# Kernel optimization log

Measured on AMD Instinct MI355X. Metric: run time of the kernel, lower is better.

The kernel has to match this reference:

```python
import jax, jax.numpy as jnp
import numpy as np

D_MODEL = 1024
N_HEADS = 16
D_HEAD = D_MODEL // N_HEADS


def setup_inputs() -> dict:
    key = jax.random.key(0)
    ks = jax.random.split(key, 16)
    B, S, D = 2, 2048, D_MODEL
    s = 1.0 / np.sqrt(D)
    inp = {
        "query": jax.random.normal(ks[0], (B, S, D), jnp.float32),
        "key": jax.random.normal(ks[1], (B, S, D), jnp.float32),
        "value": jax.random.normal(ks[2], (B, S, D), jnp.float32),
        "pos_embedding": jax.random.normal(ks[3], (B, S, D), jnp.float32),
        "Wq": jax.random.normal(ks[4], (D, D), jnp.float32) * s,
        "bq": jnp.zeros((D,), jnp.float32),
        "Wk": jax.random.normal(ks[5], (D, D), jnp.float32) * s,
        "bk": jnp.zeros((D,), jnp.float32),
        "Wv": jax.random.normal(ks[6], (D, D), jnp.float32) * s,
        "bv": jnp.zeros((D,), jnp.float32),
        "Wpos": jax.random.normal(ks[7], (D, D), jnp.float32) * s,
        "u_bias": jax.random.normal(ks[8], (N_HEADS, D_HEAD), jnp.float32) * s,
        "v_bias": jax.random.normal(ks[9], (N_HEADS, D_HEAD), jnp.float32) * s,
        "Wout": jax.random.normal(ks[10], (D, D), jnp.float32) * s,
        "bout": jnp.zeros((D,), jnp.float32),
    }
    return inp


def _rel_shift(pos_score):
    # Transformer-XL relative shift: pad one zero column, reshape, drop first row.
    B, H, S1, S2 = pos_score.shape
    zeros = jnp.zeros((B, H, S1, 1), pos_score.dtype)
    padded = jnp.concatenate([zeros, pos_score], axis=-1)  # [B,H,S1,S2+1]
    padded = padded.reshape(B, H, S2 + 1, S1)
    return padded[:, :, 1:].reshape(B, H, S1, S2)


def reference(query, key, value, pos_embedding, Wq, bq, Wk, bk, Wv, bv, Wpos, u_bias, v_bias, Wout, bout):
    B, S, D = query.shape
    H, dh = N_HEADS, D_HEAD
    q = (query @ Wq + bq).reshape(B, S, H, dh)            # [B,S,H,dh]
    k = (key @ Wk + bk).reshape(B, S, H, dh)              # [B,S,H,dh]
    v = (value @ Wv + bv).reshape(B, S, H, dh)            # [B,S,H,dh]
    p = (pos_embedding @ Wpos).reshape(B, S, H, dh)       # [B,S,H,dh]

    content_score = jnp.einsum('bqhd,bkhd->bhqk', q + u_bias, k)
    pos_score = jnp.einsum('bqhd,bkhd->bhqk', q + v_bias, p)
    pos_score = _rel_shift(pos_score)

    score = (content_score + pos_score) / jnp.asarray(np.sqrt(D), score_dtype := content_score.dtype)
    attn = jax.nn.softmax(score, axis=-1)                 # [B,H,S,S]
    context = jnp.einsum('bhqk,bkhd->bqhd', attn, v).reshape(B, S, D)
    out = context @ Wout + bout
    return out, attn
```

## Files before the change

### kernel.cpp

```cpp
#include <hip/hip_runtime.h>

#define S_LEN 2048
#define DM    1024
#define NH    16
#define DH    64
#define BATCH 2
#define S2    ((size_t)S_LEN * S_LEN)

typedef _Float16 half_t;
typedef _Float16 f16x8 __attribute__((ext_vector_type(8)));
typedef _Float16 f16x4 __attribute__((ext_vector_type(4)));
typedef float    f32x4 __attribute__((ext_vector_type(4)));

__device__ __forceinline__ void gll16(const void* g, void* l) {
  __builtin_amdgcn_global_load_lds(
      (const __attribute__((address_space(1))) void*)g,
      (__attribute__((address_space(3))) void*)l, 16, 0, 0);
}

__device__ __forceinline__ void stage_gll(half_t* lds, const half_t* src, int stride) {
  const int t = threadIdx.x, w = t >> 6, lane = t & 63;
  const int c1 = lane & 7, r8 = lane >> 3;
#pragma unroll
  for (int it = 0; it < 4; ++it) {
    int r = w * 32 + it * 8 + r8;
    const half_t* g = src + (size_t)r * stride + ((c1 ^ r8) << 3);
    gll16(g, lds + (size_t)w * 2048 + it * 512);
  }
}

__device__ __forceinline__ void mfma_block(const half_t* At, const half_t* Bt,
                                           int w, int lane, f32x4 acc[2][8]) {
  const int grp = lane >> 4, li = lane & 15;
#pragma unroll
  for (int ks = 0; ks < 2; ++ks) {
    const int chunk = ks * 4 + grp;
    f16x8 a[2], b[8];
#pragma unroll
    for (int fr = 0; fr < 2; ++fr) {
      int r = w * 32 + fr * 16 + li;
      a[fr] = *(const f16x8*)&At[(size_t)(r * 8 + (chunk ^ (r & 7))) * 8];
    }
#pragma unroll
    for (int fc = 0; fc < 8; ++fc) {
      int r = fc * 16 + li;
      b[fc] = *(const f16x8*)&Bt[(size_t)(r * 8 + (chunk ^ (r & 7))) * 8];
    }
#pragma unroll
    for (int fr = 0; fr < 2; ++fr)
#pragma unroll
      for (int fc = 0; fc < 8; ++fc)
        acc[fr][fc] = __builtin_amdgcn_mfma_f32_16x16x32_f16(a[fr], b[fc], acc[fr][fc], 0, 0, 0);
  }
}

template<typename ST>
__device__ __forceinline__ void load8s(const ST* p, float* o) {
  if constexpr (sizeof(ST) == 2) {
    f16x8 v = *(const f16x8*)p;
#pragma unroll
    for (int e = 0; e < 8; ++e) o[e] = (float)v[e];
  } else {
    const float4* q = (const float4*)p;
    float4 a = q[0], b = q[1];
    o[0]=a.x; o[1]=a.y; o[2]=a.z; o[3]=a.w; o[4]=b.x; o[5]=b.y; o[6]=b.z; o[7]=b.w;
  }
}

struct AArgs { const float* src[4]; half_t* dst[4]; };

__global__ __launch_bounds__(256) void a2h(AArgs a, half_t* zbuf) {
  if (blockIdx.x == 0 && blockIdx.y == 0 && threadIdx.x < 8) {
    float4 z = {0.f, 0.f, 0.f, 0.f};
    ((float4*)zbuf)[threadIdx.x] = z;
  }
  const float* s = a.src[blockIdx.y];
  half_t* d = a.dst[blockIdx.y];
  size_t i = ((size_t)blockIdx.x * 256 + threadIdx.x) * 8;
  float4 v0 = *(const float4*)(s + i), v1 = *(const float4*)(s + i + 4);
  f16x8 h;
  h[0]=(half_t)v0.x; h[1]=(half_t)v0.y; h[2]=(half_t)v0.z; h[3]=(half_t)v0.w;
  h[4]=(half_t)v1.x; h[5]=(half_t)v1.y; h[6]=(half_t)v1.z; h[7]=(half_t)v1.w;
  *(f16x8*)(d + i) = h;
}

struct WArgs { const float* src[5]; half_t* dst[5]; };

__global__ __launch_bounds__(256) void wconv(WArgs wa) {
  __shared__ float T[64][65];
  const float* W = wa.src[blockIdx.z];
  half_t* D = wa.dst[blockIdx.z];
  const int k0 = blockIdx.x * 64, n0 = blockIdx.y * 64;
  const int t = threadIdx.x;
#pragma unroll
  for (int it = 0; it < 4; ++it) {
    int idx = t + it * 256; int r = idx >> 4, c4 = (idx & 15) * 4;
    float4 v = *(const float4*)(W + (size_t)(k0 + r) * DM + n0 + c4);
    T[r][c4] = v.x; T[r][c4 + 1] = v.y; T[r][c4 + 2] = v.z; T[r][c4 + 3] = v.w;
  }
  __syncthreads();
#pragma unroll
  for (int it = 0; it < 2; ++it) {
    int idx = t + it * 256; int n = idx >> 3, kc = (idx & 7) * 8;
    f16x8 o;
#pragma unroll
    for (int e = 0; e < 8; ++e) o[e] = (half_t)T[kc + e][n];
    *(f16x8*)&D[(size_t)(n0 + n) * DM + k0 + kc] = o;
  }
}

struct GArgs {
  const half_t* A[4];  const half_t* Bt[4];
  const float* ba[4]; const float* bu[4]; const float* bv[4];
  half_t* oa[4]; half_t* ob[4]; float* of[4];
};

template<bool F32OUT>
__global__ __launch_bounds__(256) void gemm_k(GArgs g, int K) {
  __shared__ __align__(16) half_t At[2][128 * 64];
  __shared__ __align__(16) half_t Bt[2][128 * 64];
  const int z = blockIdx.z;
  const half_t* A = g.A[z];
  const half_t* B = g.Bt[z];
  const int n0 = blockIdx.x * 128, m0 = blockIdx.y * 128;
  const int t = threadIdx.x, w = t >> 6, lane = t & 63;
  const f32x4 zf = {0.f, 0.f, 0.f, 0.f};
  f32x4 acc[2][8];
#pragma unroll
  for (int i = 0; i < 2; ++i)
#pragma unroll
    for (int j = 0; j < 8; ++j) acc[i][j] = zf;

  stage_gll(At[0], A + (size_t)m0 * K, K);
  stage_gll(Bt[0], B + (size_t)n0 * K, K);
  __syncthreads();
  int cur = 0;
  for (int k0 = 0; k0 < K; k0 += 64) {
    int nk = k0 + 64;
    if (nk < K) {
      stage_gll(At[cur ^ 1], A + (size_t)m0 * K + nk, K);
      stage_gll(Bt[cur ^ 1], B + (size_t)n0 * K + nk, K);
    }
    mfma_block(At[cur], Bt[cur], w, lane, acc);
    __syncthreads();
    cur ^= 1;
  }
  const int grp = lane >> 4, li = lane & 15;
#pragma unroll
  for (int fr = 0; fr < 2; ++fr)
#pragma unroll
    for (int fc = 0; fc < 8; ++fc)
#pragma unroll
      for (int r = 0; r < 4; ++r) {
        int row = m0 + w * 32 + fr * 16 + grp * 4 + r;
        int col = n0 + fc * 16 + li;
        float v = acc[fr][fc][r];
        if (g.ba[z]) v += g.ba[z][col];
        if constexpr (F32OUT) {
          g.of[z][(size_t)row * DM + col] = v;
        } else {
          float v1 = v + (g.bu[z] ? g.bu[z][col] : 0.f);
          g.oa[z][(size_t)row * DM + col] = (half_t)v1;
          if (g.ob[z]) g.ob[z][(size_t)row * DM + col] = (half_t)(v + g.bv[z][col]);
        }
      }
}

__global__ __launch_bounds__(256) void vtrans(const half_t* vp, half_t* vT) {
  __shared__ half_t T[64][72];
  const int s0 = blockIdx.x * 64, h = blockIdx.y, b = blockIdx.z;
  const int t = threadIdx.x;
#pragma unroll
  for (int it = 0; it < 2; ++it) {
    int idx = t + it * 256; int s = idx >> 3, c = idx & 7;
    uint4 v = *(const uint4*)(vp + ((size_t)(b * S_LEN + s0 + s)) * DM + h * DH + c * 8);
    *(uint4*)&T[s][c * 8] = v;
  }
  __syncthreads();
  half_t* dst = vT + ((size_t)(b * NH + h)) * DH * S_LEN;
#pragma unroll
  for (int it = 0; it < 2; ++it) {
    int idx = t + it * 256; int d = idx >> 3, sc = (idx & 7) * 8;
    f16x8 o;
#pragma unroll
    for (int e = 0; e < 8; ++e) o[e] = T[sc + e][d];
    *(f16x8*)&dst[(size_t)d * S_LEN + s0 + sc] = o;
  }
}

template<typename ST>
__global__ __launch_bounds__(512, 4) void score_fused(
    const half_t* __restrict__ qu_, const half_t* __restrict__ qv_,
    const half_t* __restrict__ kp_, const half_t* __restrict__ pp_,
    const half_t* __restrict__ zbuf, ST* __restrict__ sc, float* __restrict__ part)
{
  __shared__ __align__(16) half_t RegA[32768];
  __shared__ __align__(16) half_t QV[128 * 64];
  half_t* QU = RegA;
  half_t* Kt = RegA + 8192;
  half_t* Pb = RegA + 16384;
  half_t* Mf = RegA;

  const int bh = blockIdx.z, b = bh >> 4, h = bh & 15;
  const int kt = blockIdx.x, qt = blockIdx.y;
  const int i0 = qt * 128, k0 = kt * 128;
  const int base = 1920 + k0 - i0;
  const int t = threadIdx.x, w = t >> 6, lane = t & 63;
  const int grp = lane >> 4, li = lane & 15;

  {
    const half_t* srcA = qu_ + ((size_t)(b * S_LEN + i0)) * DM + h * DH;
    const half_t* srcB = kp_ + ((size_t)(b * S_LEN + k0)) * DM + h * DH;
    const half_t* srcQ = qv_ + ((size_t)(b * S_LEN + i0)) * DM + h * DH;
#pragma unroll
    for (int p = 0; p < 2; ++p) {
      int cidx = t + p * 512; int r = cidx >> 3, c = cidx & 7;
      size_t off = (size_t)r * DM + ((c ^ (r & 7)) << 3);
      gll16(srcA + off, QU + (size_t)cidx * 8);
      gll16(srcB + off, Kt + (size_t)cidx * 8);
      gll16(srcQ + off, QV + (size_t)cidx * 8);
    }
  }
#pragma unroll
  for (int p = 0; p < 4; ++p) {
    int cidx = t + p * 512; int e = cidx >> 3, c = cidx & 7;
    int jv = base + e; if (jv >= S_LEN + 1) jv -= (S_LEN + 1);
    const half_t* src = (jv == S_LEN)
        ? (zbuf + ((c ^ (e & 7)) << 3))
        : (pp_ + ((size_t)(b * S_LEN + jv)) * DM + h * DH + ((c ^ (e & 7)) << 3));
    gll16(src, Pb + (size_t)cidx * 8);
  }

  f16x8 aq[2];
  {
    int r128 = i0 + 128; if (r128 > S_LEN - 1) r128 = S_LEN - 1;
    const half_t* q128p = qv_ + ((size_t)(b * S_LEN + r128)) * DM + h * DH;
    aq[0] = *(const f16x8*)(q128p + (0 * 4 + grp) * 8);
    aq[1] = *(const f16x8*)(q128p + (1 * 4 + grp) * 8);
  }
  __syncthreads();

  const f32x4 zf = {0.f, 0.f, 0.f, 0.f};
  f32x4 acc_c[8];
#pragma unroll
  for (int j = 0; j < 8; ++j) acc_c[j] = zf;
#pragma unroll
  for (int kk = 0; kk < 2; ++kk) {
    const int chunk = kk * 4 + grp;
    int ra = w * 16 + li;
    f16x8 a = *(const f16x8*)&QU[(size_t)(ra * 8 + (chunk ^ (ra & 7))) * 8];
#pragma unroll
    for (int fc = 0; fc < 8; ++fc) {
      int rb = fc * 16 + li;
      f16x8 bf = *(const f16x8*)&Kt[(size_t)(rb * 8 + (chunk ^ (rb & 7))) * 8];
      acc_c[fc] = __builtin_amdgcn_mfma_f32_16x16x32_f16(a, bf, acc_c[fc], 0, 0, 0);
    }
  }
  f16x8 bm[2][2];
#pragma unroll
  for (int kk = 0; kk < 2; ++kk)
#pragma unroll
    for (int eci = 0; eci < 2; ++eci) {
      int rb = (w + eci * 8) * 16 + li;
      bm[kk][eci] = *(const f16x8*)&Pb[(size_t)(rb * 8 + ((kk * 4 + grp) ^ (rb & 7))) * 8];
    }
  __syncthreads();

  for (int rf = 0; rf < 8; ++rf) {
    f32x4 am[2] = {zf, zf};
#pragma unroll
    for (int kk = 0; kk < 2; ++kk) {
      int ra = rf * 16 + li;
      f16x8 a = *(const f16x8*)&QV[(size_t)(ra * 8 + ((kk * 4 + grp) ^ (ra & 7))) * 8];
#pragma unroll
      for (int eci = 0; eci < 2; ++eci)
        am[eci] = __builtin_amdgcn_mfma_f32_16x16x32_f16(a, bm[kk][eci], am[eci], 0, 0, 0);
    }
#pragma unroll
    for (int eci = 0; eci < 2; ++eci) {
      int ec = w + eci * 8;
      if (!(ec == 15 && li == 15)) {
        f16x4 hv;
#pragma unroll
        for (int r = 0; r < 4; ++r) hv[r] = (half_t)am[eci][r];
        *(f16x4*)&Mf[(size_t)(((ec * 8 + rf) * 4 + grp) * 64 + li * 4)] = hv;
      }
    }
  }

  {
    f32x4 am0 = zf;
#pragma unroll
    for (int kk = 0; kk < 2; ++kk)
      am0 = __builtin_amdgcn_mfma_f32_16x16x32_f16(aq[kk], bm[kk][0], am0, 0, 0, 0);
    if (grp == 0) {
      int e = w * 16 + li;
      Mf[(size_t)(((120 + (e >> 4)) * 4 + ((e >> 2) & 3)) * 64 + 60 + (e & 3))] = (half_t)am0[0];
    }
  }
  __syncthreads();

  ST* sb = sc + (size_t)bh * S2;
  float lsum[4] = {0.f, 0.f, 0.f, 0.f};
#pragma unroll
  for (int fc = 0; fc < 8; ++fc) {
#pragma unroll
    for (int rr = 0; rr < 4; ++rr) {
      int q = w * 16 + grp * 4 + rr;
      int k = fc * 16 + li;
      int e = k - q + 127;
      int jv = base + e;
      int dlt = (jv >= S_LEN + 1) ? 1 : 0;
      int rM = q + dlt;
      float mval;
      if (rM < 128) {
        int ec = e >> 4, ei = e & 15, rf = rM >> 4, ri = rM & 15;
        mval = (float)Mf[(size_t)(((ec * 8 + rf) * 4 + (ri >> 2)) * 64 + ei * 4 + (ri & 3))];
      } else {
        mval = (float)Mf[(size_t)(((120 + (e >> 4)) * 4 + ((e >> 2) & 3)) * 64 + 60 + (e & 3))];
      }
      float s = (acc_c[fc][rr] + mval) * 0.03125f;
      float ev = __expf(s);
      sb[(size_t)(i0 + q) * S_LEN + k0 + k] = (ST)ev;
      lsum[rr] += ev;
    }
  }
#pragma unroll
  for (int rr = 0; rr < 4; ++rr) {
    float v = lsum[rr];
#pragma unroll
    for (int d = 1; d < 16; d <<= 1) v += __shfl_xor(v, d);
    if (li == 0)
      part[((size_t)bh * S_LEN + i0 + w * 16 + grp * 4 + rr) * 16 + kt] = v;
  }
}

template<typename ST>
__global__ __launch_bounds__(256) void av_attn(const ST* sc, const half_t* vT, const float* part,
                                               float* attn, half_t* ctx) {
  __shared__ __align__(16) half_t Vt[2][64 * 128];
  __shared__ float Ls[128];
  const int bh = blockIdx.y, b = bh >> 4, h = bh & 15;
  const int q0 = blockIdx.x * 128;
  const int t = threadIdx.x;
  if (t < 128) {
    const float* pp = part + ((size_t)bh * S_LEN + q0 + t) * 16;
    float L = 0.f;
#pragma unroll
    for (int k = 0; k < 16; ++k) L += pp[k];
    Ls[t] = 1.f / L;
  }
  const ST* sb = sc + (size_t)bh * S2;
  float* ab = attn + (size_t)bh * S2;
  const half_t* vb = vT + (size_t)bh * (DH * S_LEN);
  const int w = t >> 6, lane = t & 63, grp = lane >> 4, li = lane & 15;
  const int c1 = lane & 15, d4 = lane >> 4;
  const f32x4 zf = {0.f, 0.f, 0.f, 0.f};
  f32x4 acc[2][4];
#pragma unroll
  for (int i = 0; i < 2; ++i)
#pragma unroll
    for (int j = 0; j < 4; ++j) acc[i][j] = zf;

#pragma unroll
  for (int it = 0; it < 4; ++it) {
    int d = w * 16 + it * 4 + d4;
    gll16(vb + (size_t)d * S_LEN + ((c1 ^ (d & 15)) << 3), Vt[0] + (size_t)w * 2048 + it * 512);
  }
  __syncthreads();
  int cur = 0;

  for (int kt = 0; kt < 16; ++kt) {
    if (kt + 1 < 16) {
#pragma unroll
      for (int it = 0; it < 4; ++it) {
        int d = w * 16 + it * 4 + d4;
        gll16(vb + (size_t)d * S_LEN + (kt + 1) * 128 + ((c1 ^ (d & 15)) << 3),
              Vt[cur ^ 1] + (size_t)w * 2048 + it * 512);
      }
    }
#pragma unroll
    for (int ks = 0; ks < 4; ++ks) {
      f16x8 pa[2];
#pragma unroll
      for (int fr = 0; fr < 2; ++fr) {
        int r128 = w * 32 + fr * 16 + li;
        int row = q0 + r128;
        int col = kt * 128 + ks * 32 + grp * 8;
        float sv[8];
        load8s(&sb[(size_t)row * S_LEN + col], sv);
        float rL = Ls[r128];
#pragma unroll
        for (int e = 0; e < 8; ++e) sv[e] *= rL;
        float4* dst = (float4*)&ab[(size_t)row * S_LEN + col];
        float4 w0 = {sv[0], sv[1], sv[2], sv[3]};
        float4 w1 = {sv[4], sv[5], sv[6], sv[7]};
        dst[0] = w0; dst[1] = w1;
        f16x8 ph;
#pragma unroll
        for (int e = 0; e < 8; ++e) ph[e] = (half_t)sv[e];
        pa[fr] = ph;
      }
      f16x8 bf[4];
#pragma unroll
      for (int fc = 0; fc < 4; ++fc) {
        int d = fc * 16 + li; int chunk = ks * 4 + grp;
        bf[fc] = *(const f16x8*)&Vt[cur][(size_t)(d * 16 + (chunk ^ (d & 15))) * 8];
      }
#pragma unroll
      for (int fr = 0; fr < 2; ++fr)
#pragma unroll
        for (int fc = 0; fc < 4; ++fc)
          acc[fr][fc] = __builtin_amdgcn_mfma_f32_16x16x32_f16(pa[fr], bf[fc], acc[fr][fc], 0, 0, 0);
    }
    __syncthreads();
    cur ^= 1;
  }
#pragma unroll
  for (int fr = 0; fr < 2; ++fr)
#pragma unroll
    for (int fc = 0; fc < 4; ++fc)
#pragma unroll
      for (int r = 0; r < 4; ++r) {
        int q = q0 + w * 32 + fr * 16 + grp * 4 + r;
        int d = fc * 16 + li;
        ctx[((size_t)(b * S_LEN + q)) * DM + h * DH + d] = (half_t)acc[fr][fc][r];
      }
}

extern "C" void kernel_launch(void* const* d_in, const int* in_sizes, int n_in,
                              void* d_out, int out_size, void* d_ws, size_t ws_size,
                              hipStream_t stream) {
  (void)in_sizes; (void)n_in; (void)out_size;

  const float* query  = (const float*)d_in[0];
  const float* key    = (const float*)d_in[1];
  const float* value  = (const float*)d_in[2];
  const float* pos    = (const float*)d_in[3];
  const float* Wq     = (const float*)d_in[4];
  const float* bq     = (const float*)d_in[5];
  const float* Wk     = (const float*)d_in[6];
  const float* bk     = (const float*)d_in[7];
  const float* Wv     = (const float*)d_in[8];
  const float* bv     = (const float*)d_in[9];
  const float* Wpos   = (const float*)d_in[10];
  const float* u_bias = (const float*)d_in[11];
  const float* v_bias = (const float*)d_in[12];
  const float* Wout   = (const float*)d_in[13];
  const float* bout   = (const float*)d_in[14];

  float* out  = (float*)d_out;
  float* attn = out + (size_t)BATCH * S_LEN * DM;

  char* ws = (char*)d_ws;
  half_t* Wt   = (half_t*)(ws);
  half_t* Af16 = (half_t*)(ws + 10485760);
  float*  part = (float*)(ws + 10485760);
  half_t* qu   = (half_t*)(ws + 44040192);
  half_t* qv   = (half_t*)(ws + 52428800);
  half_t* kp   = (half_t*)(ws + 60817408);
  half_t* pp   = (half_t*)(ws + 69206016);
  half_t* vp   = (half_t*)(ws + 77594624);
  half_t* vT   = (half_t*)(ws + 85983232);
  half_t* ctx  = (half_t*)(ws + 77594624);
  half_t* zbuf = (half_t*)(ws + 94371840);
  half_t* scH  = (half_t*)(ws + 94375936);
  const bool fast = ws_size >= (size_t)94375936 + (size_t)BATCH * NH * S2 * 2;

  dim3 blk(256);

  AArgs aa;
  aa.src[0] = query; aa.src[1] = key; aa.src[2] = value; aa.src[3] = pos;
  for (int i = 0; i < 4; ++i) aa.dst[i] = Af16 + (size_t)i * BATCH * S_LEN * DM;
  a2h<<<dim3(2048, 4), blk, 0, stream>>>(aa, zbuf);

  WArgs wa;
  wa.src[0] = Wq; wa.src[1] = Wk; wa.src[2] = Wv; wa.src[3] = Wpos; wa.src[4] = Wout;
  for (int i = 0; i < 5; ++i) wa.dst[i] = Wt + (size_t)i * DM * DM;
  wconv<<<dim3(16, 16, 5), blk, 0, stream>>>(wa);

  GArgs ga{};
  for (int i = 0; i < 4; ++i) {
    ga.A[i]  = Af16 + (size_t)i * BATCH * S_LEN * DM;
    ga.Bt[i] = Wt + (size_t)i * DM * DM;
  }
  ga.ba[0] = bq; ga.ba[1] = bk; ga.ba[2] = bv; ga.ba[3] = nullptr;
  ga.bu[0] = u_bias; ga.bv[0] = v_bias;
  ga.oa[0] = qu; ga.oa[1] = kp; ga.oa[2] = vp; ga.oa[3] = pp;
  ga.ob[0] = qv;
  gemm_k<false><<<dim3(8, 32, 4), blk, 0, stream>>>(ga, DM);

  vtrans<<<dim3(32, 16, 2), blk, 0, stream>>>(vp, vT);

  dim3 g_sc(16, 16, 32);
  dim3 blk5(512);
  if (fast) {
    score_fused<half_t><<<g_sc, blk5, 0, stream>>>(qu, qv, kp, pp, zbuf, scH, part);
    av_attn<half_t><<<dim3(16, 32), blk, 0, stream>>>(scH, vT, part, attn, ctx);
  } else {
    float* scF = attn;
    score_fused<float><<<g_sc, blk5, 0, stream>>>(qu, qv, kp, pp, zbuf, scF, part);
    av_attn<float><<<dim3(16, 32), blk, 0, stream>>>(scF, vT, part, attn, ctx);
  }

  GArgs go{};
  go.A[0] = ctx; go.Bt[0] = Wt + (size_t)4 * DM * DM;
  go.ba[0] = bout; go.of[0] = out;
  gemm_k<true><<<dim3(8, 32, 1), blk, 0, stream>>>(go, DM);
}
```

Before: 542.7 us.

## Merge activation and weight conversion kernels; single-buffer GEMM shared-memory staging

```diff
diff --git a/kernel.cpp b/kernel.cpp
--- a/kernel.cpp
+++ b/kernel.cpp
@@ -67,45 +67,49 @@
   }
 }
 
-struct AArgs { const float* src[4]; half_t* dst[4]; };
-
-__global__ __launch_bounds__(256) void a2h(AArgs a, half_t* zbuf) {
-  if (blockIdx.x == 0 && blockIdx.y == 0 && threadIdx.x < 8) {
-    float4 z = {0.f, 0.f, 0.f, 0.f};
-    ((float4*)zbuf)[threadIdx.x] = z;
-  }
-  const float* s = a.src[blockIdx.y];
-  half_t* d = a.dst[blockIdx.y];
-  size_t i = ((size_t)blockIdx.x * 256 + threadIdx.x) * 8;
-  float4 v0 = *(const float4*)(s + i), v1 = *(const float4*)(s + i + 4);
-  f16x8 h;
-  h[0]=(half_t)v0.x; h[1]=(half_t)v0.y; h[2]=(half_t)v0.z; h[3]=(half_t)v0.w;
-  h[4]=(half_t)v1.x; h[5]=(half_t)v1.y; h[6]=(half_t)v1.z; h[7]=(half_t)v1.w;
-  *(f16x8*)(d + i) = h;
-}
-
-struct WArgs { const float* src[5]; half_t* dst[5]; };
-
-__global__ __launch_bounds__(256) void wconv(WArgs wa) {
+struct PArgs {
+  const float* asrc[4]; half_t* adst[4];
+  const float* wsrc[5]; half_t* wdst[5];
+};
+
+__global__ __launch_bounds__(256) void prep(PArgs pa, half_t* zbuf) {
   __shared__ float T[64][65];
-  const float* W = wa.src[blockIdx.z];
-  half_t* D = wa.dst[blockIdx.z];
-  const int k0 = blockIdx.x * 64, n0 = blockIdx.y * 64;
-  const int t = threadIdx.x;
-#pragma unroll
-  for (int it = 0; it < 4; ++it) {
-    int idx = t + it * 256; int r = idx >> 4, c4 = (idx & 15) * 4;
-    float4 v = *(const float4*)(W + (size_t)(k0 + r) * DM + n0 + c4);
-    T[r][c4] = v.x; T[r][c4 + 1] = v.y; T[r][c4 + 2] = v.z; T[r][c4 + 3] = v.w;
-  }
-  __syncthreads();
-#pragma unroll
-  for (int it = 0; it < 2; ++it) {
-    int idx = t + it * 256; int n = idx >> 3, kc = (idx & 7) * 8;
-    f16x8 o;
-#pragma unroll
-    for (int e = 0; e < 8; ++e) o[e] = (half_t)T[kc + e][n];
-    *(f16x8*)&D[(size_t)(n0 + n) * DM + k0 + kc] = o;
+  const int bx = blockIdx.x, t = threadIdx.x;
+  if (bx < 8192) {
+    if (bx == 0 && t < 8) {
+      float4 z = {0.f, 0.f, 0.f, 0.f};
+      ((float4*)zbuf)[t] = z;
+    }
+    const int mat = bx >> 11, blk = bx & 2047;
+    const float* s = pa.asrc[mat];
+    half_t* d = pa.adst[mat];
+    size_t i = ((size_t)blk * 256 + t) * 8;
+    float4 v0 = *(const float4*)(s + i), v1 = *(const float4*)(s + i + 4);
+    f16x8 h;
+    h[0]=(half_t)v0.x; h[1]=(half_t)v0.y; h[2]=(half_t)v0.z; h[3]=(half_t)v0.w;
+    h[4]=(half_t)v1.x; h[5]=(half_t)v1.y; h[6]=(half_t)v1.z; h[7]=(half_t)v1.w;
+    *(f16x8*)(d + i) = h;
+  } else {
+    const int idx = bx - 8192;
+    const int z = idx >> 8, rem = idx & 255;
+    const int k0 = (rem & 15) * 64, n0 = (rem >> 4) * 64;
+    const float* W = pa.wsrc[z];
+    half_t* D = pa.wdst[z];
+#pragma unroll
+    for (int it = 0; it < 4; ++it) {
+      int id2 = t + it * 256; int r = id2 >> 4, c4 = (id2 & 15) * 4;
+      float4 v = *(const float4*)(W + (size_t)(k0 + r) * DM + n0 + c4);
+      T[r][c4] = v.x; T[r][c4 + 1] = v.y; T[r][c4 + 2] = v.z; T[r][c4 + 3] = v.w;
+    }
+    __syncthreads();
+#pragma unroll
+    for (int it = 0; it < 2; ++it) {
+      int id2 = t + it * 256; int n = id2 >> 3, kc = (id2 & 7) * 8;
+      f16x8 o;
+#pragma unroll
+      for (int e = 0; e < 8; ++e) o[e] = (half_t)T[kc + e][n];
+      *(f16x8*)&D[(size_t)(n0 + n) * DM + k0 + kc] = o;
+    }
   }
 }
 
@@ -117,8 +121,8 @@
 
 template<bool F32OUT>
 __global__ __launch_bounds__(256) void gemm_k(GArgs g, int K) {
-  __shared__ __align__(16) half_t At[2][128 * 64];
-  __shared__ __align__(16) half_t Bt[2][128 * 64];
+  __shared__ __align__(16) half_t At[128 * 64];
+  __shared__ __align__(16) half_t Bt[128 * 64];
   const int z = blockIdx.z;
   const half_t* A = g.A[z];
   const half_t* B = g.Bt[z];
@@ -131,19 +135,12 @@
 #pragma unroll
     for (int j = 0; j < 8; ++j) acc[i][j] = zf;
 
-  stage_gll(At[0], A + (size_t)m0 * K, K);
-  stage_gll(Bt[0], B + (size_t)n0 * K, K);
-  __syncthreads();
-  int cur = 0;
   for (int k0 = 0; k0 < K; k0 += 64) {
-    int nk = k0 + 64;
-    if (nk < K) {
-      stage_gll(At[cur ^ 1], A + (size_t)m0 * K + nk, K);
-      stage_gll(Bt[cur ^ 1], B + (size_t)n0 * K + nk, K);
-    }
-    mfma_block(At[cur], Bt[cur], w, lane, acc);
+    stage_gll(At, A + (size_t)m0 * K + k0, K);
+    stage_gll(Bt, B + (size_t)n0 * K + k0, K);
     __syncthreads();
-    cur ^= 1;
+    mfma_block(At, Bt, w, lane, acc);
+    __syncthreads();
   }
   const int grp = lane >> 4, li = lane & 15;
 #pragma unroll
@@ -469,15 +466,12 @@
 
   dim3 blk(256);
 
-  AArgs aa;
-  aa.src[0] = query; aa.src[1] = key; aa.src[2] = value; aa.src[3] = pos;
-  for (int i = 0; i < 4; ++i) aa.dst[i] = Af16 + (size_t)i * BATCH * S_LEN * DM;
-  a2h<<<dim3(2048, 4), blk, 0, stream>>>(aa, zbuf);
-
-  WArgs wa;
-  wa.src[0] = Wq; wa.src[1] = Wk; wa.src[2] = Wv; wa.src[3] = Wpos; wa.src[4] = Wout;
-  for (int i = 0; i < 5; ++i) wa.dst[i] = Wt + (size_t)i * DM * DM;
-  wconv<<<dim3(16, 16, 5), blk, 0, stream>>>(wa);
+  PArgs pa;
+  pa.asrc[0] = query; pa.asrc[1] = key; pa.asrc[2] = value; pa.asrc[3] = pos;
+  for (int i = 0; i < 4; ++i) pa.adst[i] = Af16 + (size_t)i * BATCH * S_LEN * DM;
+  pa.wsrc[0] = Wq; pa.wsrc[1] = Wk; pa.wsrc[2] = Wv; pa.wsrc[3] = Wpos; pa.wsrc[4] = Wout;
+  for (int i = 0; i < 5; ++i) pa.wdst[i] = Wt + (size_t)i * DM * DM;
+  prep<<<dim3(8192 + 1280), blk, 0, stream>>>(pa, zbuf);
 
   GArgs ga{};
   for (int i = 0; i < 4; ++i) {
```

Measured after the change: 548.7 us. About the same (+1.1%).
